# Kernel optimization log

Measured on AMD Instinct MI355X. Metric: run time of the kernel, lower is better.

Reference implementation:

```python
import jax, jax.numpy as jnp
import numpy as np

B, T, D, S, K = 4, 4096, 1024, 2048, 8

def _l2norm(v, axis=-1, eps=1e-12):
    # matches torch F.normalize: v / max(||v||, eps)
    n = jnp.sqrt(jnp.sum(v * v, axis=axis, keepdims=True))
    return v / jnp.maximum(n, eps)

def setup_inputs() -> dict:
    key = jax.random.key(0)
    ks = jax.random.split(key, 9)
    H = D // 2
    return {
        "x": jax.random.normal(ks[0], (B, T, D), dtype=jnp.float32),
        "memory_keys": jax.random.normal(ks[1], (S, D), dtype=jnp.float32) * 0.02,
        "memory_values": jax.random.normal(ks[2], (S, D), dtype=jnp.float32) * 0.02,
        "Wq": jax.random.normal(ks[3], (D, D), dtype=jnp.float32) * (1.0 / np.sqrt(D)),
        "Wo": jax.random.normal(ks[4], (D, D), dtype=jnp.float32) * (1.0 / np.sqrt(D)),
        "gW1": jax.random.normal(ks[5], (H, 2 * D), dtype=jnp.float32) * (1.0 / np.sqrt(2 * D)),
        "gb1": jnp.zeros((H,), dtype=jnp.float32),
        "gW2": jax.random.normal(ks[6], (1, H), dtype=jnp.float32) * (1.0 / np.sqrt(H)),
        "gb2": jnp.zeros((1,), dtype=jnp.float32),
    }

def reference(x, memory_keys, memory_values, Wq, Wo, gW1, gb1, gW2, gb2):
    # query projection (Linear, no bias): y = x @ W.T
    queries = jnp.einsum('btd,ed->bte', x, Wq)
    keys_norm = _l2norm(memory_keys)          # [S, D]
    queries_norm = _l2norm(queries)           # [B, T, D]
    # cosine similarities [B, T, S]
    sims = jnp.einsum('btd,sd->bts', queries_norm, keys_norm)
    topk_sims, topk_idx = jax.lax.top_k(sims, K)      # [B, T, K]
    topk_w = jax.nn.softmax(topk_sims, axis=-1)       # [B, T, K]
    topk_vals = memory_values[topk_idx]               # [B, T, K, D]
    retrieved = jnp.einsum('btk,btkd->btd', topk_w, topk_vals)
    retrieved = jnp.einsum('btd,ed->bte', retrieved, Wo)
    gate_in = jnp.concatenate([x, retrieved], axis=-1)           # [B, T, 2D]
    h = jax.nn.gelu(jnp.einsum('btc,hc->bth', gate_in, gW1) + gb1, approximate=False)
    gate = jax.nn.sigmoid(jnp.einsum('bth,oh->bto', h, gW2) + gb2)  # [B, T, 1]
    return x + gate * retrieved
```

## Files before the change

### kernel.cpp

```cpp
#include <hip/hip_runtime.h>
#include <math.h>

#define NROWS 16384
#define DDIM  1024
#define SKEYS 2048
#define KTOP  8
#define HDIM  512

typedef short  s16x8 __attribute__((ext_vector_type(8)));
typedef float  f32x4 __attribute__((ext_vector_type(4)));

#define GL16(g, l) __builtin_amdgcn_global_load_lds(                      \
    (const __attribute__((address_space(1))) void*)(g),                   \
    (__attribute__((address_space(3))) void*)(l), 16, 0, 0)

__device__ __forceinline__ float wave_sum(float v) {
#pragma unroll
    for (int off = 32; off > 0; off >>= 1) v += __shfl_xor(v, off, 64);
    return v;
}

__device__ __forceinline__ unsigned short f2bf(float f) {
    union { float f; unsigned u; } c; c.f = f;
    unsigned u = c.u;
    unsigned r = (u + 0x7FFFu + ((u >> 16) & 1u)) >> 16;
    return (unsigned short)r;
}

__device__ __forceinline__ float gelu_exact(float v) {
    return 0.5f * v * (1.0f + erff(v * 0.7071067811865475f));
}

__device__ __forceinline__ ushort4 cvt4(float4 v) {
    ushort4 o;
    o.x = f2bf(v.x); o.y = f2bf(v.y); o.z = f2bf(v.z); o.w = f2bf(v.w);
    return o;
}

__global__ __launch_bounds__(256) void prep_kernel(
        const float* __restrict__ x,   const float* __restrict__ Wq,
        const float* __restrict__ Wo,  const float* __restrict__ mv,
        const float* __restrict__ gW1, const float* __restrict__ mk,
        unsigned short* __restrict__ x_bf, unsigned short* __restrict__ wqcat,
        unsigned short* __restrict__ wo_bf, unsigned short* __restrict__ mv_bf,
        unsigned short* __restrict__ gw1b, unsigned short* __restrict__ kn) {
    int bid = blockIdx.x, t = threadIdx.x;
    {
        float4 v = ((const float4*)(mk + (size_t)bid * DDIM))[t];
        float ss = v.x * v.x + v.y * v.y + v.z * v.z + v.w * v.w;
        ss = wave_sum(ss);
        __shared__ float wsum[4];
        if ((t & 63) == 0) wsum[t >> 6] = ss;
        __syncthreads();
        float tot = wsum[0] + wsum[1] + wsum[2] + wsum[3];
        float sc = 1.0f / fmaxf(sqrtf(tot), 1e-12f);
        float4 o = make_float4(v.x * sc, v.y * sc, v.z * sc, v.w * sc);
        ((ushort4*)(kn + (size_t)bid * DDIM))[t] = cvt4(o);
    }
    int gid = bid * 256 + t, stride = gridDim.x * 256;
    for (int i = gid; i < NROWS * DDIM / 4; i += stride)
        ((ushort4*)x_bf)[i] = cvt4(((const float4*)x)[i]);
    for (int i = gid; i < DDIM * DDIM / 4; i += stride)
        ((ushort4*)wqcat)[i] = cvt4(((const float4*)Wq)[i]);
    for (int i = gid; i < HDIM * 2 * DDIM / 4; i += stride) {
        float4 v = ((const float4*)gW1)[i];
        int r = i >> 9, c4 = i & 511;
        if (c4 < 256) ((ushort4*)wqcat)[DDIM * DDIM / 4 + r * 256 + c4] = cvt4(v);
        else          ((ushort4*)gw1b)[r * 256 + (c4 - 256)] = cvt4(v);
    }
    for (int i = gid; i < DDIM * DDIM / 4; i += stride)
        ((ushort4*)wo_bf)[i] = cvt4(((const float4*)Wo)[i]);
    for (int i = gid; i < SKEYS * DDIM / 4; i += stride)
        ((ushort4*)mv_bf)[i] = cvt4(((const float4*)mv)[i]);
}

struct GArg {
    const unsigned short* A;
    const unsigned short* B;
    unsigned short* C;
    unsigned short* C2;
    float* qpart;
    int Ncols, N2cols, nsplit, gx, nblocks, mode;
};

__global__ __launch_bounds__(256, 3) void dualgemm(GArg g0, GArg g1, int split) {
    __shared__ __align__(16) unsigned short As[2][4096];
    __shared__ __align__(16) unsigned short Bs[2][4096];

    int tid = threadIdx.x, l = tid & 63, wid = tid >> 6;
    bool first = ((int)blockIdx.x < split);
    GArg g = first ? g0 : g1;
    int bid = first ? blockIdx.x : blockIdx.x - split;
    int cpx = g.nblocks >> 3;
    int sbid = (bid & 7) * cpx + (bid >> 3);
    int m0 = (sbid / g.gx) * 128;
    int n0 = (sbid % g.gx) * 128;

    int wr = wid >> 1, wc = wid & 1;
    constexpr int NT = 32;

    f32x4 acc[4][4];
#pragma unroll
    for (int i = 0; i < 4; ++i)
#pragma unroll
        for (int j = 0; j < 4; ++j) acc[i][j] = (f32x4){0.f, 0.f, 0.f, 0.f};

    int srow   = tid >> 2;
    int schunk = (tid & 3) ^ ((srow >> 1) & 3);
    int offA[2], offB[2];
#pragma unroll
    for (int i = 0; i < 2; ++i) {
        offA[i] = (m0 + i * 64 + srow) * 1024;
        offB[i] = (n0 + i * 64 + srow) * 1024;
    }
    int ldsU = wid * 512;

#define STAGE(bsel, kt_)                                                       \
    do {                                                                       \
        int gk_ = (kt_) * 32 + schunk * 8;                                     \
        _Pragma("unroll")                                                      \
        for (int i_ = 0; i_ < 2; ++i_) {                                       \
            GL16(g.A + offA[i_] + gk_, &As[bsel][i_ * 2048 + ldsU]);           \
            GL16(g.B + offB[i_] + gk_, &Bs[bsel][i_ * 2048 + ldsU]);           \
        }                                                                      \
    } while (0)

    STAGE(0, 0);

    int frow = l & 15;
    int fp   = (l >> 4) ^ ((frow >> 1) & 3);
    int aoff = (wr * 64 + frow) * 32 + fp * 8;
    int boff = (wc * 64 + frow) * 32 + fp * 8;

#pragma unroll 2
    for (int kt = 0; kt < NT; ++kt) {
        int b = kt & 1;
        if (kt + 1 < NT) {
            STAGE(b ^ 1, kt + 1);
            asm volatile("s_waitcnt vmcnt(4)" ::: "memory");
        } else {
            asm volatile("s_waitcnt vmcnt(0)" ::: "memory");
        }
        __builtin_amdgcn_s_barrier();
        asm volatile("" ::: "memory");

        s16x8 af[4], bfr[4];
#pragma unroll
        for (int mf = 0; mf < 4; ++mf)
            af[mf] = *(const s16x8*)&As[b][aoff + mf * 512];
#pragma unroll
        for (int nf = 0; nf < 4; ++nf)
            bfr[nf] = *(const s16x8*)&Bs[b][boff + nf * 512];

        __builtin_amdgcn_s_setprio(1);
#pragma unroll
        for (int mf = 0; mf < 4; ++mf)
#pragma unroll
            for (int nf = 0; nf < 4; ++nf)
                acc[mf][nf] = __builtin_amdgcn_mfma_f32_16x16x32_bf16(
                    af[mf], bfr[nf], acc[mf][nf], 0, 0, 0);
        __builtin_amdgcn_s_setprio(0);
        asm volatile("" ::: "memory");
        __builtin_amdgcn_s_barrier();
        asm volatile("" ::: "memory");
    }
#undef STAGE

    unsigned short* cptr = g.C;
    int nc = g.Ncols, cb = n0;
    bool qreg = (g.mode == 2);
    if (g.mode == 2 && n0 >= g.nsplit) {
        cptr = g.C2; nc = g.N2cols; cb = n0 - g.nsplit; qreg = false;
    }

    int crow = (l >> 4) << 2;
    int ccol = l & 15;
    float rs[4][4];
#pragma unroll
    for (int i = 0; i < 4; ++i)
#pragma unroll
        for (int j = 0; j < 4; ++j) rs[i][j] = 0.f;

#pragma unroll
    for (int mf = 0; mf < 4; ++mf) {
        int gr = m0 + wr * 64 + mf * 16 + crow;
#pragma unroll
        for (int nf = 0; nf < 4; ++nf) {
            int gc = cb + wc * 64 + nf * 16 + ccol;
            f32x4 v = acc[mf][nf];
#pragma unroll
            for (int r2 = 0; r2 < 4; ++r2) {
                float o = v[r2];
                unsigned short sv = f2bf(o);
                if (g.mode == 3)
                    sv = sv ^ ((sv & 0x8000) ? 0xFFFFu : 0x8000u);
                cptr[(size_t)(gr + r2) * nc + gc] = sv;
                if (qreg) rs[mf][r2] += o * o;
            }
        }
    }
    if (qreg) {
        int slot = (n0 >> 7) * 2 + wc;
#pragma unroll
        for (int mf = 0; mf < 4; ++mf)
#pragma unroll
            for (int r2 = 0; r2 < 4; ++r2) {
                float s = rs[mf][r2];
                s += __shfl_xor(s, 1, 64);
                s += __shfl_xor(s, 2, 64);
                s += __shfl_xor(s, 4, 64);
                s += __shfl_xor(s, 8, 64);
                if ((l & 15) == 0)
                    g.qpart[(size_t)slot * NROWS +
                            (m0 + wr * 64 + mf * 16 + (l >> 4) * 4 + r2)] = s;
            }
    }
}

#define CED(k, i, j)                                                      \
    { unsigned mx_ = k[i] > k[j] ? k[i] : k[j];                           \
      unsigned mn_ = k[i] > k[j] ? k[j] : k[i];                           \
      k[i] = mx_; k[j] = mn_; }

__device__ __forceinline__ void sort8d(unsigned* k) {
    CED(k,0,1) CED(k,2,3) CED(k,4,5) CED(k,6,7)
    CED(k,0,2) CED(k,1,3) CED(k,4,6) CED(k,5,7)
    CED(k,1,2) CED(k,5,6)
    CED(k,0,4) CED(k,1,5) CED(k,2,6) CED(k,3,7)
    CED(k,2,4) CED(k,3,5)
    CED(k,1,2) CED(k,3,4) CED(k,5,6)
}

__device__ __forceinline__ void bclean8d(unsigned* t) {
    CED(t,0,4) CED(t,1,5) CED(t,2,6) CED(t,3,7)
    CED(t,0,2) CED(t,1,3) CED(t,4,6) CED(t,5,7)
    CED(t,0,1) CED(t,2,3) CED(t,4,5) CED(t,6,7)
}

__device__ __forceinline__ void merge8d(unsigned* a, const unsigned* b) {
    unsigned t[8];
#pragma unroll
    for (int i = 0; i < 8; ++i) t[i] = a[i] > b[7 - i] ? a[i] : b[7 - i];
    bclean8d(t);
#pragma unroll
    for (int i = 0; i < 8; ++i) a[i] = t[i];
}

__global__ __launch_bounds__(256) void mega_kernel(
        const float* __restrict__ qpart,
        const unsigned short* __restrict__ sims,
        const unsigned short* __restrict__ x_bf,
        const unsigned short* __restrict__ xg1,
        const unsigned short* __restrict__ mvo,
        const unsigned short* __restrict__ mvog,
        const float* __restrict__ gb1, const float* __restrict__ gW2,
        const float* __restrict__ gb2, float* __restrict__ out) {
    int wid = threadIdx.x >> 6, l = threadIdx.x & 63;
    int row = blockIdx.x * 4 + wid;

    const unsigned short* sr = sims + (size_t)row * SKEYS;
    uint4 raw0 = *(const uint4*)(sr + 0 * 512 + l * 8);
    uint4 raw1 = *(const uint4*)(sr + 1 * 512 + l * 8);
    uint4 raw2 = *(const uint4*)(sr + 2 * 512 + l * 8);
    uint4 raw3 = *(const uint4*)(sr + 3 * 512 + l * 8);
    const unsigned short* xr = x_bf + (size_t)row * DDIM + l * 16;
    uint4 x0 = *(const uint4*)xr, x1 = *(const uint4*)(xr + 8);
    uint4 xg = *(const uint4*)(xg1 + (size_t)row * HDIM + l * 8);

    float ssq = 0.f;
#pragma unroll
    for (int j = 0; j < 16; ++j) ssq += qpart[(size_t)j * NROWS + row];
    float qs = 1.0f / fmaxf(sqrtf(ssq), 1e-12f);

    unsigned key[32];
    {
        unsigned rw[16] = {raw0.x, raw0.y, raw0.z, raw0.w,
                           raw1.x, raw1.y, raw1.z, raw1.w,
                           raw2.x, raw2.y, raw2.z, raw2.w,
                           raw3.x, raw3.y, raw3.z, raw3.w};
#pragma unroll
        for (int c = 0; c < 4; ++c)
#pragma unroll
            for (int q2 = 0; q2 < 4; ++q2) {
                unsigned v = rw[c * 4 + q2];
                unsigned bi0 = (unsigned)(c * 512 + l * 8 + q2 * 2);
                key[c * 8 + q2 * 2]     = ((v & 0xFFFFu) << 16) | bi0;
                key[c * 8 + q2 * 2 + 1] = (v & 0xFFFF0000u) | (bi0 + 1);
            }
    }
    sort8d(key); sort8d(key + 8); sort8d(key + 16); sort8d(key + 24);
    merge8d(key, key + 8);
    merge8d(key + 16, key + 24);
    merge8d(key, key + 16);

#pragma unroll
    for (int off = 1; off <= 32; off <<= 1) {
        unsigned br[8];
#pragma unroll
        for (int i = 0; i < 8; ++i)
            br[i] = (unsigned)__shfl_xor((int)key[7 - i], off, 64);
        unsigned t[8];
#pragma unroll
        for (int i = 0; i < 8; ++i) t[i] = key[i] > br[i] ? key[i] : br[i];
        bclean8d(t);
#pragma unroll
        for (int i = 0; i < 8; ++i) key[i] = t[i];
    }

    float ov[8]; int oi[8];
#pragma unroll
    for (int j = 0; j < 8; ++j) {
        oi[j] = (int)(key[j] & 0xFFFFu);
        unsigned short ks = (unsigned short)(key[j] >> 16);
        unsigned short sv = ks ^ ((ks & 0x8000) ? 0x8000u : 0xFFFFu);
        ov[j] = __uint_as_float(((unsigned)sv) << 16);
    }
    float w[KTOP];
    float m = ov[0] * qs, ssum = 0.f;
#pragma unroll
    for (int j = 0; j < 8; ++j) { w[j] = expf(ov[j] * qs - m); ssum += w[j]; }
    float sinv = 1.0f / ssum;
#pragma unroll
    for (int j = 0; j < 8; ++j) w[j] *= sinv;

    float r2[16], hp[8];
#pragma unroll
    for (int j = 0; j < 16; ++j) r2[j] = 0.f;
#pragma unroll
    for (int j = 0; j < 8; ++j) hp[j] = 0.f;
#pragma unroll
    for (int k = 0; k < KTOP; ++k) {
        float wk = w[k];
        const unsigned short* mo = mvo + (size_t)oi[k] * DDIM + l * 16;
        uint4 a0 = *(const uint4*)mo;
        uint4 a1 = *(const uint4*)(mo + 8);
        const unsigned short* mg = mvog + (size_t)oi[k] * HDIM + l * 8;
        uint4 g0 = *(const uint4*)mg;
        unsigned aw[8] = {a0.x, a0.y, a0.z, a0.w, a1.x, a1.y, a1.z, a1.w};
#pragma unroll
        for (int j = 0; j < 8; ++j) {
            r2[2 * j]     += wk * __uint_as_float(aw[j] << 16);
            r2[2 * j + 1] += wk * __uint_as_float(aw[j] & 0xffff0000u);
        }
        unsigned gw[4] = {g0.x, g0.y, g0.z, g0.w};
#pragma unroll
        for (int j = 0; j < 4; ++j) {
            hp[2 * j]     += wk * __uint_as_float(gw[j] << 16);
            hp[2 * j + 1] += wk * __uint_as_float(gw[j] & 0xffff0000u);
        }
    }
    unsigned xgw[4] = {xg.x, xg.y, xg.z, xg.w};
    float p = 0.f;
#pragma unroll
    for (int j = 0; j < 4; ++j) {
        float h0 = gelu_exact(hp[2 * j] + __uint_as_float(xgw[j] << 16)
                              + gb1[l * 8 + 2 * j]);
        float h1 = gelu_exact(hp[2 * j + 1] + __uint_as_float(xgw[j] & 0xffff0000u)
                              + gb1[l * 8 + 2 * j + 1]);
        p += h0 * gW2[l * 8 + 2 * j] + h1 * gW2[l * 8 + 2 * j + 1];
    }
    p = wave_sum(p);
    float gate = 1.0f / (1.0f + expf(-(p + gb2[0])));
    unsigned xw[8] = {x0.x, x0.y, x0.z, x0.w, x1.x, x1.y, x1.z, x1.w};
    float o[16];
#pragma unroll
    for (int j = 0; j < 8; ++j) {
        o[2 * j]     = __uint_as_float(xw[j] << 16)         + gate * r2[2 * j];
        o[2 * j + 1] = __uint_as_float(xw[j] & 0xffff0000u) + gate * r2[2 * j + 1];
    }
    float4* po = (float4*)(out + (size_t)row * DDIM + l * 16);
    po[0] = make_float4(o[0], o[1], o[2], o[3]);
    po[1] = make_float4(o[4], o[5], o[6], o[7]);
    po[2] = make_float4(o[8], o[9], o[10], o[11]);
    po[3] = make_float4(o[12], o[13], o[14], o[15]);
}

extern "C" void kernel_launch(void* const* d_in, const int* in_sizes, int n_in,
                              void* d_out, int out_size, void* d_ws, size_t ws_size,
                              hipStream_t stream) {
    (void)in_sizes; (void)n_in; (void)out_size; (void)ws_size;
    const float* x   = (const float*)d_in[0];
    const float* mk  = (const float*)d_in[1];
    const float* mv  = (const float*)d_in[2];
    const float* Wq  = (const float*)d_in[3];
    const float* Wo  = (const float*)d_in[4];
    const float* gW1 = (const float*)d_in[5];
    const float* gb1 = (const float*)d_in[6];
    const float* gW2 = (const float*)d_in[7];
    const float* gb2 = (const float*)d_in[8];
    float* out = (float*)d_out;

    char* w = (char*)d_ws;
    unsigned short* x_bf    = (unsigned short*)w;  w += (size_t)NROWS * DDIM * 2;
    unsigned short* q_bf    = (unsigned short*)w;  w += (size_t)NROWS * DDIM * 2;
    unsigned short* xg1_bf  = (unsigned short*)w;  w += (size_t)NROWS * HDIM * 2;
    unsigned short* kn_bf   = (unsigned short*)w;  w += (size_t)SKEYS * DDIM * 2;
    unsigned short* wqcat   = (unsigned short*)w;  w += (size_t)(DDIM + HDIM) * DDIM * 2;
    unsigned short* gw1b_bf = (unsigned short*)w;  w += (size_t)HDIM * DDIM * 2;
    unsigned short* wo_bf   = (unsigned short*)w;  w += (size_t)DDIM * DDIM * 2;
    unsigned short* mv_bf   = (unsigned short*)w;  w += (size_t)SKEYS * DDIM * 2;
    unsigned short* mvo_bf  = (unsigned short*)w;  w += (size_t)SKEYS * DDIM * 2;
    unsigned short* mvog_bf = (unsigned short*)w;  w += (size_t)SKEYS * HDIM * 2;
    unsigned short* sims    = (unsigned short*)w;  w += (size_t)NROWS * SKEYS * 2;
    float* qpart = (float*)w;                      w += (size_t)16 * NROWS * 4;

    prep_kernel<<<SKEYS, 256, 0, stream>>>(x, Wq, Wo, mv, gW1, mk,
                                           x_bf, wqcat, wo_bf, mv_bf, gw1b_bf, kn_bf);

    {
        GArg gq; gq.A = x_bf;  gq.B = wqcat; gq.C = q_bf;  gq.C2 = xg1_bf;
        gq.qpart = qpart; gq.Ncols = DDIM; gq.N2cols = HDIM; gq.nsplit = DDIM;
        gq.gx = 12; gq.nblocks = 1536; gq.mode = 2;
        GArg gm; gm.A = mv_bf; gm.B = wo_bf; gm.C = mvo_bf; gm.C2 = nullptr;
        gm.qpart = nullptr; gm.Ncols = DDIM; gm.N2cols = 0; gm.nsplit = 0;
        gm.gx = 8; gm.nblocks = 128; gm.mode = 0;
        dualgemm<<<1664, 256, 0, stream>>>(gq, gm, 1536);
    }

    {
        GArg gs; gs.A = q_bf;   gs.B = kn_bf;   gs.C = sims;    gs.C2 = nullptr;
        gs.qpart = nullptr; gs.Ncols = SKEYS; gs.N2cols = 0; gs.nsplit = 0;
        gs.gx = 16; gs.nblocks = 2048; gs.mode = 3;
        GArg gg; gg.A = mvo_bf; gg.B = gw1b_bf; gg.C = mvog_bf; gg.C2 = nullptr;
        gg.qpart = nullptr; gg.Ncols = HDIM; gg.N2cols = 0; gg.nsplit = 0;
        gg.gx = 4; gg.nblocks = 64; gg.mode = 0;
        dualgemm<<<2112, 256, 0, stream>>>(gs, gg, 2048);
    }

    mega_kernel<<<NROWS / 4, 256, 0, stream>>>(
        qpart, sims, x_bf, xg1_bf, mvo_bf, mvog_bf, gb1, gW2, gb2, out);
}
```

Measured before the change: 264.3 us.

## Enlarge dual GEMM tiles to 256x256 with 8 waves and interleaved staging

Moves the bf16 GEMM kernel from 128x128 tiles with 4 waves and K-step 32 to 256x256 tiles with 8 waves and K-step 64. The next stage's global-to-LDS loads are split into four parts interleaved between the MFMA groups. This raises arithmetic intensity and cuts the number of barrier-separated iterations, aiming to reduce global/LDS traffic per FLOP. In exchange it uses 128KB of LDS per block and 128 accumulator registers per thread, which limits occupancy, and it leaves fewer blocks, which may cause tail effects on the small side GEMMs.

```diff
diff --git a/kernel.cpp b/kernel.cpp
--- a/kernel.cpp
+++ b/kernel.cpp
@@ -83,9 +83,9 @@
     int Ncols, N2cols, nsplit, gx, nblocks, mode;
 };
 
-__global__ __launch_bounds__(256, 3) void dualgemm(GArg g0, GArg g1, int split) {
-    __shared__ __align__(16) unsigned short As[2][4096];
-    __shared__ __align__(16) unsigned short Bs[2][4096];
+__global__ __launch_bounds__(512, 2) void dualgemm(GArg g0, GArg g1, int split) {
+    __shared__ __align__(16) unsigned short As[2][16384];
+    __shared__ __align__(16) unsigned short Bs[2][16384];
 
     int tid = threadIdx.x, l = tid & 63, wid = tid >> 6;
     bool first = ((int)blockIdx.x < split);
@@ -93,51 +93,43 @@
     int bid = first ? blockIdx.x : blockIdx.x - split;
     int cpx = g.nblocks >> 3;
     int sbid = (bid & 7) * cpx + (bid >> 3);
-    int m0 = (sbid / g.gx) * 128;
-    int n0 = (sbid % g.gx) * 128;
-
-    int wr = wid >> 1, wc = wid & 1;
-    constexpr int NT = 32;
-
-    f32x4 acc[4][4];
-#pragma unroll
-    for (int i = 0; i < 4; ++i)
+    int m0 = (sbid / g.gx) * 256;
+    int n0 = (sbid % g.gx) * 256;
+
+    int wm = wid >> 2, wn = wid & 3;
+
+    f32x4 acc[8][4];
+#pragma unroll
+    for (int i = 0; i < 8; ++i)
 #pragma unroll
         for (int j = 0; j < 4; ++j) acc[i][j] = (f32x4){0.f, 0.f, 0.f, 0.f};
 
-    int srow   = tid >> 2;
-    int schunk = (tid & 3) ^ ((srow >> 1) & 3);
-    int offA[2], offB[2];
-#pragma unroll
-    for (int i = 0; i < 2; ++i) {
-        offA[i] = (m0 + i * 64 + srow) * 1024;
-        offB[i] = (n0 + i * 64 + srow) * 1024;
-    }
+    int srw = wid * 8 + (l >> 3);
+    int sch = (l & 7) ^ ((l >> 3) & 7);
     int ldsU = wid * 512;
 
-#define STAGE(bsel, kt_)                                                       \
+#define SPART(bsel, kt_, p_)                                                   \
     do {                                                                       \
-        int gk_ = (kt_) * 32 + schunk * 8;                                     \
-        _Pragma("unroll")                                                      \
-        for (int i_ = 0; i_ < 2; ++i_) {                                       \
-            GL16(g.A + offA[i_] + gk_, &As[bsel][i_ * 2048 + ldsU]);           \
-            GL16(g.B + offB[i_] + gk_, &Bs[bsel][i_ * 2048 + ldsU]);           \
-        }                                                                      \
+        int gk_ = (kt_) * 64 + sch * 8;                                        \
+        GL16(g.A + (size_t)(m0 + (p_) * 64 + srw) * 1024 + gk_,                \
+             &As[bsel][(p_) * 4096 + ldsU]);                                   \
+        GL16(g.B + (size_t)(n0 + (p_) * 64 + srw) * 1024 + gk_,                \
+             &Bs[bsel][(p_) * 4096 + ldsU]);                                   \
     } while (0)
 
-    STAGE(0, 0);
-
-    int frow = l & 15;
-    int fp   = (l >> 4) ^ ((frow >> 1) & 3);
-    int aoff = (wr * 64 + frow) * 32 + fp * 8;
-    int boff = (wc * 64 + frow) * 32 + fp * 8;
-
-#pragma unroll 2
-    for (int kt = 0; kt < NT; ++kt) {
+    int aBase = (wm * 128 + (l & 15)) * 64;
+    int bBase = (wn * 64 + (l & 15)) * 64;
+    int ch0 = (((l >> 4)) ^ (l & 7)) * 8;
+    int ch1 = ((4 + (l >> 4)) ^ (l & 7)) * 8;
+
+    SPART(0, 0, 0); SPART(0, 0, 1); SPART(0, 0, 2); SPART(0, 0, 3);
+
+    for (int kt = 0; kt < 16; ++kt) {
         int b = kt & 1;
-        if (kt + 1 < NT) {
-            STAGE(b ^ 1, kt + 1);
-            asm volatile("s_waitcnt vmcnt(4)" ::: "memory");
+        bool more = (kt + 1 < 16);
+        if (more) {
+            SPART(b ^ 1, kt + 1, 0);
+            asm volatile("s_waitcnt vmcnt(2)" ::: "memory");
         } else {
             asm volatile("s_waitcnt vmcnt(0)" ::: "memory");
         }
@@ -146,12 +138,11 @@
 
         s16x8 af[4], bfr[4];
 #pragma unroll
-        for (int mf = 0; mf < 4; ++mf)
-            af[mf] = *(const s16x8*)&As[b][aoff + mf * 512];
-#pragma unroll
         for (int nf = 0; nf < 4; ++nf)
-            bfr[nf] = *(const s16x8*)&Bs[b][boff + nf * 512];
-
+            bfr[nf] = *(const s16x8*)&Bs[b][bBase + nf * 1024 + ch0];
+#pragma unroll
+        for (int mf = 0; mf < 4; ++mf)
+            af[mf] = *(const s16x8*)&As[b][aBase + mf * 1024 + ch0];
         __builtin_amdgcn_s_setprio(1);
 #pragma unroll
         for (int mf = 0; mf < 4; ++mf)
@@ -160,11 +151,54 @@
                 acc[mf][nf] = __builtin_amdgcn_mfma_f32_16x16x32_bf16(
                     af[mf], bfr[nf], acc[mf][nf], 0, 0, 0);
         __builtin_amdgcn_s_setprio(0);
+        if (more) SPART(b ^ 1, kt + 1, 1);
+
+#pragma unroll
+        for (int mf = 0; mf < 4; ++mf)
+            af[mf] = *(const s16x8*)&As[b][aBase + (mf + 4) * 1024 + ch0];
+        __builtin_amdgcn_s_setprio(1);
+#pragma unroll
+        for (int mf = 0; mf < 4; ++mf)
+#pragma unroll
+            for (int nf = 0; nf < 4; ++nf)
+                acc[mf + 4][nf] = __builtin_amdgcn_mfma_f32_16x16x32_bf16(
+                    af[mf], bfr[nf], acc[mf + 4][nf], 0, 0, 0);
+        __builtin_amdgcn_s_setprio(0);
+        if (more) SPART(b ^ 1, kt + 1, 2);
+
+#pragma unroll
+        for (int nf = 0; nf < 4; ++nf)
+            bfr[nf] = *(const s16x8*)&Bs[b][bBase + nf * 1024 + ch1];
+#pragma unroll
+        for (int mf = 0; mf < 4; ++mf)
+            af[mf] = *(const s16x8*)&As[b][aBase + mf * 1024 + ch1];
+        __builtin_amdgcn_s_setprio(1);
+#pragma unroll
+        for (int mf = 0; mf < 4; ++mf)
+#pragma unroll
+            for (int nf = 0; nf < 4; ++nf)
+                acc[mf][nf] = __builtin_amdgcn_mfma_f32_16x16x32_bf16(
+                    af[mf], bfr[nf], acc[mf][nf], 0, 0, 0);
+        __builtin_amdgcn_s_setprio(0);
+        if (more) SPART(b ^ 1, kt + 1, 3);
+
+#pragma unroll
+        for (int mf = 0; mf < 4; ++mf)
+            af[mf] = *(const s16x8*)&As[b][aBase + (mf + 4) * 1024 + ch1];
+        __builtin_amdgcn_s_setprio(1);
+#pragma unroll
+        for (int mf = 0; mf < 4; ++mf)
+#pragma unroll
+            for (int nf = 0; nf < 4; ++nf)
+                acc[mf + 4][nf] = __builtin_amdgcn_mfma_f32_16x16x32_bf16(
+                    af[mf], bfr[nf], acc[mf + 4][nf], 0, 0, 0);
+        __builtin_amdgcn_s_setprio(0);
+
         asm volatile("" ::: "memory");
         __builtin_amdgcn_s_barrier();
         asm volatile("" ::: "memory");
     }
-#undef STAGE
+#undef SPART
 
     unsigned short* cptr = g.C;
     int nc = g.Ncols, cb = n0;
@@ -175,44 +209,39 @@
 
     int crow = (l >> 4) << 2;
     int ccol = l & 15;
-    float rs[4][4];
-#pragma unroll
-    for (int i = 0; i < 4; ++i)
-#pragma unroll
-        for (int j = 0; j < 4; ++j) rs[i][j] = 0.f;
-
-#pragma unroll
-    for (int mf = 0; mf < 4; ++mf) {
-        int gr = m0 + wr * 64 + mf * 16 + crow;
+#pragma unroll
+    for (int mf = 0; mf < 8; ++mf) {
+        int gr = m0 + wm * 128 + mf * 16 + crow;
 #pragma unroll
         for (int nf = 0; nf < 4; ++nf) {
-            int gc = cb + wc * 64 + nf * 16 + ccol;
+            int gc = cb + wn * 64 + nf * 16 + ccol;
             f32x4 v = acc[mf][nf];
 #pragma unroll
             for (int r2 = 0; r2 < 4; ++r2) {
-                float o = v[r2];
-                unsigned short sv = f2bf(o);
+                unsigned short sv = f2bf(v[r2]);
                 if (g.mode == 3)
                     sv = sv ^ ((sv & 0x8000) ? 0xFFFFu : 0x8000u);
                 cptr[(size_t)(gr + r2) * nc + gc] = sv;
-                if (qreg) rs[mf][r2] += o * o;
             }
         }
     }
     if (qreg) {
-        int slot = (n0 >> 7) * 2 + wc;
-#pragma unroll
-        for (int mf = 0; mf < 4; ++mf)
+        int slot = (n0 >> 6) + wn;
+#pragma unroll
+        for (int mf = 0; mf < 8; ++mf)
 #pragma unroll
             for (int r2 = 0; r2 < 4; ++r2) {
-                float s = rs[mf][r2];
+                float s = acc[mf][0][r2] * acc[mf][0][r2]
+                        + acc[mf][1][r2] * acc[mf][1][r2]
+                        + acc[mf][2][r2] * acc[mf][2][r2]
+                        + acc[mf][3][r2] * acc[mf][3][r2];
                 s += __shfl_xor(s, 1, 64);
                 s += __shfl_xor(s, 2, 64);
                 s += __shfl_xor(s, 4, 64);
                 s += __shfl_xor(s, 8, 64);
                 if ((l & 15) == 0)
                     g.qpart[(size_t)slot * NROWS +
-                            (m0 + wr * 64 + mf * 16 + (l >> 4) * 4 + r2)] = s;
+                            (m0 + wm * 128 + mf * 16 + (l >> 4) * 4 + r2)] = s;
             }
     }
 }
@@ -410,21 +439,21 @@
     {
         GArg gq; gq.A = x_bf;  gq.B = wqcat; gq.C = q_bf;  gq.C2 = xg1_bf;
         gq.qpart = qpart; gq.Ncols = DDIM; gq.N2cols = HDIM; gq.nsplit = DDIM;
-        gq.gx = 12; gq.nblocks = 1536; gq.mode = 2;
+        gq.gx = 6; gq.nblocks = 384; gq.mode = 2;
         GArg gm; gm.A = mv_bf; gm.B = wo_bf; gm.C = mvo_bf; gm.C2 = nullptr;
         gm.qpart = nullptr; gm.Ncols = DDIM; gm.N2cols = 0; gm.nsplit = 0;
-        gm.gx = 8; gm.nblocks = 128; gm.mode = 0;
-        dualgemm<<<1664, 256, 0, stream>>>(gq, gm, 1536);
+        gm.gx = 4; gm.nblocks = 32; gm.mode = 0;
+        dualgemm<<<416, 512, 0, stream>>>(gq, gm, 384);
     }
 
     {
         GArg gs; gs.A = q_bf;   gs.B = kn_bf;   gs.C = sims;    gs.C2 = nullptr;
         gs.qpart = nullptr; gs.Ncols = SKEYS; gs.N2cols = 0; gs.nsplit = 0;
-        gs.gx = 16; gs.nblocks = 2048; gs.mode = 3;
+        gs.gx = 8; gs.nblocks = 512; gs.mode = 3;
         GArg gg; gg.A = mvo_bf; gg.B = gw1b_bf; gg.C = mvog_bf; gg.C2 = nullptr;
         gg.qpart = nullptr; gg.Ncols = HDIM; gg.N2cols = 0; gg.nsplit = 0;
-        gg.gx = 4; gg.nblocks = 64; gg.mode = 0;
-        dualgemm<<<2112, 256, 0, stream>>>(gs, gg, 2048);
+        gg.gx = 2; gg.nblocks = 16; gg.mode = 0;
+        dualgemm<<<528, 512, 0, stream>>>(gs, gg, 512);
     }
 
     mega_kernel<<<NROWS / 4, 256, 0, stream>>>(
```

New measurement: 311.0 us. 17.7% more time.

## Fold Wq into normalized keys so sims come straight from x

Applied to the files above, without the earlier changes.

Precomputes kn·Wq (a 2048x1024 by 1024x1024 GEMM) so that similarities are computed as x·(kn Wq)^T. This removes the 16384x1024 query materialization and its re-read in a second GEMM. One fused GEMM now produces the sims, the query norms (via the Wq rows in the concatenated B) and the xg1 projection, with per-region epilogues. The cost is extra GEMM work on the small matrices and a transpose of Wq in the prep kernel. Numerics change because the bf16 rounding now happens on the folded key matrix instead of on q.

```diff
diff --git a/kernel.cpp b/kernel.cpp
--- a/kernel.cpp
+++ b/kernel.cpp
@@ -41,10 +41,12 @@
         const float* __restrict__ x,   const float* __restrict__ Wq,
         const float* __restrict__ Wo,  const float* __restrict__ mv,
         const float* __restrict__ gW1, const float* __restrict__ mk,
-        unsigned short* __restrict__ x_bf, unsigned short* __restrict__ wqcat,
-        unsigned short* __restrict__ wo_bf, unsigned short* __restrict__ mv_bf,
-        unsigned short* __restrict__ gw1b, unsigned short* __restrict__ kn) {
+        unsigned short* __restrict__ x_bf, unsigned short* __restrict__ bcat,
+        unsigned short* __restrict__ wqT, unsigned short* __restrict__ wo_bf,
+        unsigned short* __restrict__ mv_bf, unsigned short* __restrict__ gw1b,
+        unsigned short* __restrict__ kn) {
     int bid = blockIdx.x, t = threadIdx.x;
+    __shared__ float tlds[64][65];
     {
         float4 v = ((const float4*)(mk + (size_t)bid * DDIM))[t];
         float ss = v.x * v.x + v.y * v.y + v.z * v.z + v.w * v.w;
@@ -57,15 +59,29 @@
         float4 o = make_float4(v.x * sc, v.y * sc, v.z * sc, v.w * sc);
         ((ushort4*)(kn + (size_t)bid * DDIM))[t] = cvt4(o);
     }
+    if (bid < 256) {
+        int d0 = (bid >> 4) * 64, e0 = (bid & 15) * 64;
+#pragma unroll
+        for (int i = 0; i < 16; ++i) {
+            int dr = i * 4 + (t >> 6);
+            tlds[dr][t & 63] = Wq[(size_t)(d0 + dr) * DDIM + e0 + (t & 63)];
+        }
+        __syncthreads();
+#pragma unroll
+        for (int i = 0; i < 16; ++i) {
+            int er = i * 4 + (t >> 6);
+            wqT[(size_t)(e0 + er) * DDIM + d0 + (t & 63)] = f2bf(tlds[t & 63][er]);
+        }
+    }
     int gid = bid * 256 + t, stride = gridDim.x * 256;
     for (int i = gid; i < NROWS * DDIM / 4; i += stride)
         ((ushort4*)x_bf)[i] = cvt4(((const float4*)x)[i]);
     for (int i = gid; i < DDIM * DDIM / 4; i += stride)
-        ((ushort4*)wqcat)[i] = cvt4(((const float4*)Wq)[i]);
+        ((ushort4*)bcat)[524288 + i] = cvt4(((const float4*)Wq)[i]);
     for (int i = gid; i < HDIM * 2 * DDIM / 4; i += stride) {
         float4 v = ((const float4*)gW1)[i];
         int r = i >> 9, c4 = i & 511;
-        if (c4 < 256) ((ushort4*)wqcat)[DDIM * DDIM / 4 + r * 256 + c4] = cvt4(v);
+        if (c4 < 256) ((ushort4*)bcat)[786432 + r * 256 + c4] = cvt4(v);
         else          ((ushort4*)gw1b)[r * 256 + (c4 - 256)] = cvt4(v);
     }
     for (int i = gid; i < DDIM * DDIM / 4; i += stride)
@@ -80,7 +96,7 @@
     unsigned short* C;
     unsigned short* C2;
     float* qpart;
-    int Ncols, N2cols, nsplit, gx, nblocks, mode;
+    int Ncols, N2cols, nsplit, nsplit2, gx, nblocks, mode;
 };
 
 __global__ __launch_bounds__(256, 3) void dualgemm(GArg g0, GArg g1, int split) {
@@ -166,46 +182,44 @@
     }
 #undef STAGE
 
+    int region = 0;
     unsigned short* cptr = g.C;
     int nc = g.Ncols, cb = n0;
-    bool qreg = (g.mode == 2);
-    if (g.mode == 2 && n0 >= g.nsplit) {
-        cptr = g.C2; nc = g.N2cols; cb = n0 - g.nsplit; qreg = false;
+    if (g.mode == 5) {
+        if (n0 < g.nsplit) region = 1;
+        else if (n0 < g.nsplit2) region = 2;
+        else { region = 3; cptr = g.C2; nc = g.N2cols; cb = n0 - g.nsplit2; }
     }
 
     int crow = (l >> 4) << 2;
     int ccol = l & 15;
-    float rs[4][4];
-#pragma unroll
-    for (int i = 0; i < 4; ++i)
-#pragma unroll
-        for (int j = 0; j < 4; ++j) rs[i][j] = 0.f;
-
-#pragma unroll
-    for (int mf = 0; mf < 4; ++mf) {
-        int gr = m0 + wr * 64 + mf * 16 + crow;
-#pragma unroll
-        for (int nf = 0; nf < 4; ++nf) {
-            int gc = cb + wc * 64 + nf * 16 + ccol;
-            f32x4 v = acc[mf][nf];
+    if (region != 2) {
+#pragma unroll
+        for (int mf = 0; mf < 4; ++mf) {
+            int gr = m0 + wr * 64 + mf * 16 + crow;
+#pragma unroll
+            for (int nf = 0; nf < 4; ++nf) {
+                int gc = cb + wc * 64 + nf * 16 + ccol;
+                f32x4 v = acc[mf][nf];
+#pragma unroll
+                for (int r2 = 0; r2 < 4; ++r2) {
+                    unsigned short sv = f2bf(v[r2]);
+                    if (region == 1)
+                        sv = sv ^ ((sv & 0x8000) ? 0xFFFFu : 0x8000u);
+                    cptr[(size_t)(gr + r2) * nc + gc] = sv;
+                }
+            }
+        }
+    } else {
+        int slot = ((n0 - g.nsplit) >> 7) * 2 + wc;
+#pragma unroll
+        for (int mf = 0; mf < 4; ++mf)
 #pragma unroll
             for (int r2 = 0; r2 < 4; ++r2) {
-                float o = v[r2];
-                unsigned short sv = f2bf(o);
-                if (g.mode == 3)
-                    sv = sv ^ ((sv & 0x8000) ? 0xFFFFu : 0x8000u);
-                cptr[(size_t)(gr + r2) * nc + gc] = sv;
-                if (qreg) rs[mf][r2] += o * o;
-            }
-        }
-    }
-    if (qreg) {
-        int slot = (n0 >> 7) * 2 + wc;
-#pragma unroll
-        for (int mf = 0; mf < 4; ++mf)
-#pragma unroll
-            for (int r2 = 0; r2 < 4; ++r2) {
-                float s = rs[mf][r2];
+                float s = acc[mf][0][r2] * acc[mf][0][r2]
+                        + acc[mf][1][r2] * acc[mf][1][r2]
+                        + acc[mf][2][r2] * acc[mf][2][r2]
+                        + acc[mf][3][r2] * acc[mf][3][r2];
                 s += __shfl_xor(s, 1, 64);
                 s += __shfl_xor(s, 2, 64);
                 s += __shfl_xor(s, 4, 64);
@@ -392,10 +406,10 @@
 
     char* w = (char*)d_ws;
     unsigned short* x_bf    = (unsigned short*)w;  w += (size_t)NROWS * DDIM * 2;
-    unsigned short* q_bf    = (unsigned short*)w;  w += (size_t)NROWS * DDIM * 2;
     unsigned short* xg1_bf  = (unsigned short*)w;  w += (size_t)NROWS * HDIM * 2;
     unsigned short* kn_bf   = (unsigned short*)w;  w += (size_t)SKEYS * DDIM * 2;
-    unsigned short* wqcat   = (unsigned short*)w;  w += (size_t)(DDIM + HDIM) * DDIM * 2;
+    unsigned short* bcat    = (unsigned short*)w;  w += (size_t)3584 * DDIM * 2;
+    unsigned short* wqT_bf  = (unsigned short*)w;  w += (size_t)DDIM * DDIM * 2;
     unsigned short* gw1b_bf = (unsigned short*)w;  w += (size_t)HDIM * DDIM * 2;
     unsigned short* wo_bf   = (unsigned short*)w;  w += (size_t)DDIM * DDIM * 2;
     unsigned short* mv_bf   = (unsigned short*)w;  w += (size_t)SKEYS * DDIM * 2;
@@ -405,26 +419,27 @@
     float* qpart = (float*)w;                      w += (size_t)16 * NROWS * 4;
 
     prep_kernel<<<SKEYS, 256, 0, stream>>>(x, Wq, Wo, mv, gW1, mk,
-                                           x_bf, wqcat, wo_bf, mv_bf, gw1b_bf, kn_bf);
+                                           x_bf, bcat, wqT_bf, wo_bf, mv_bf,
+                                           gw1b_bf, kn_bf);
 
     {
-        GArg gq; gq.A = x_bf;  gq.B = wqcat; gq.C = q_bf;  gq.C2 = xg1_bf;
-        gq.qpart = qpart; gq.Ncols = DDIM; gq.N2cols = HDIM; gq.nsplit = DDIM;
-        gq.gx = 12; gq.nblocks = 1536; gq.mode = 2;
+        GArg gk; gk.A = kn_bf; gk.B = wqT_bf; gk.C = bcat; gk.C2 = nullptr;
+        gk.qpart = nullptr; gk.Ncols = DDIM; gk.N2cols = 0;
+        gk.nsplit = 0; gk.nsplit2 = 0; gk.gx = 8; gk.nblocks = 128; gk.mode = 0;
         GArg gm; gm.A = mv_bf; gm.B = wo_bf; gm.C = mvo_bf; gm.C2 = nullptr;
-        gm.qpart = nullptr; gm.Ncols = DDIM; gm.N2cols = 0; gm.nsplit = 0;
-        gm.gx = 8; gm.nblocks = 128; gm.mode = 0;
-        dualgemm<<<1664, 256, 0, stream>>>(gq, gm, 1536);
+        gm.qpart = nullptr; gm.Ncols = DDIM; gm.N2cols = 0;
+        gm.nsplit = 0; gm.nsplit2 = 0; gm.gx = 8; gm.nblocks = 128; gm.mode = 0;
+        dualgemm<<<256, 256, 0, stream>>>(gk, gm, 128);
     }
 
     {
-        GArg gs; gs.A = q_bf;   gs.B = kn_bf;   gs.C = sims;    gs.C2 = nullptr;
-        gs.qpart = nullptr; gs.Ncols = SKEYS; gs.N2cols = 0; gs.nsplit = 0;
-        gs.gx = 16; gs.nblocks = 2048; gs.mode = 3;
+        GArg gb; gb.A = x_bf; gb.B = bcat; gb.C = sims; gb.C2 = xg1_bf;
+        gb.qpart = qpart; gb.Ncols = SKEYS; gb.N2cols = HDIM;
+        gb.nsplit = 2048; gb.nsplit2 = 3072; gb.gx = 28; gb.nblocks = 3584; gb.mode = 5;
         GArg gg; gg.A = mvo_bf; gg.B = gw1b_bf; gg.C = mvog_bf; gg.C2 = nullptr;
-        gg.qpart = nullptr; gg.Ncols = HDIM; gg.N2cols = 0; gg.nsplit = 0;
-        gg.gx = 4; gg.nblocks = 64; gg.mode = 0;
-        dualgemm<<<2112, 256, 0, stream>>>(gs, gg, 2048);
+        gg.qpart = nullptr; gg.Ncols = HDIM; gg.N2cols = 0;
+        gg.nsplit = 0; gg.nsplit2 = 0; gg.gx = 4; gg.nblocks = 64; gg.mode = 0;
+        dualgemm<<<3648, 256, 0, stream>>>(gb, gg, 3584);
     }
 
     mega_kernel<<<NROWS / 4, 256, 0, stream>>>(
```

Result: no change. 268.1 us (+1.4%).
